# Optimization experiments

Measured on AMD Instinct MI355X. Metric: run time of the kernel, lower is better.

Reference implementation:

```python
import jax, jax.numpy as jnp
import numpy as np

B, T, V, E, H = 64, 32, 32000, 512, 1024  # batch, caption len, vocab, embed, hidden


def setup_inputs() -> dict:
    key = jax.random.key(0)
    ks = jax.random.split(key, 10)
    sV = 1.0 / np.sqrt(V)   # nn.Linear init scale
    sH = 1.0 / np.sqrt(H)   # nn.LSTM init scale
    return {
        "features": jax.random.normal(ks[0], (B, E), jnp.float32),
        "captions": jax.random.randint(ks[1], (B, T), 0, V, dtype=jnp.int32),
        # embed = nn.Linear(vocab_size, embed_size): W [E, V], b [E]
        "W_embed": jax.random.uniform(ks[2], (E, V), jnp.float32, -sV, sV),
        "b_embed": jax.random.uniform(ks[3], (E,), jnp.float32, -sV, sV),
        # single-layer LSTM params, PyTorch gate order (i, f, g, o)
        "w_ih": jax.random.uniform(ks[4], (4 * H, E), jnp.float32, -sH, sH),
        "w_hh": jax.random.uniform(ks[5], (4 * H, H), jnp.float32, -sH, sH),
        "b_ih": jax.random.uniform(ks[6], (4 * H,), jnp.float32, -sH, sH),
        "b_hh": jax.random.uniform(ks[7], (4 * H,), jnp.float32, -sH, sH),
        # the torch module draws these with torch.randn at every call; made explicit here
        "h0": jax.random.normal(ks[8], (B, H), jnp.float32),
        "c0": jax.random.normal(ks[9], (B, H), jnp.float32),
    }


def _lstm(inputs, h0, c0, w_ih, w_hh, b_ih, b_hh):
    # inputs: [B, S, E] -> outputs [B, S, H]
    def step(carry, x_t):
        h, c = carry
        gates = x_t @ w_ih.T + h @ w_hh.T + (b_ih + b_hh)  # [B, 4H]
        i, f, g, o = jnp.split(gates, 4, axis=-1)
        c = jax.nn.sigmoid(f) * c + jax.nn.sigmoid(i) * jnp.tanh(g)
        h = jax.nn.sigmoid(o) * jnp.tanh(c)
        return (h, c), h

    _, hs = jax.lax.scan(step, (h0, c0), jnp.transpose(inputs, (1, 0, 2)))
    return jnp.transpose(hs, (1, 0, 2))


def reference(features, captions, W_embed, b_embed, w_ih, w_hh, b_ih, b_hh, h0, c0):
    # Faithful to the original: expand captions to dense one-hot [B, T, V]
    # and push through the Linear layer (the exact wasteful op pattern under study).
    onehot = jax.nn.one_hot(captions, V, dtype=jnp.float32)       # [B, T, V]
    emb = jnp.einsum("btv,ev->bte", onehot, W_embed) + b_embed     # [B, T, E]
    inputs = jnp.concatenate([features[:, None, :], emb], axis=1)  # [B, T+1, E]
    return _lstm(inputs, h0, c0, w_ih, w_hh, b_ih, b_hh)           # [B, T+1, H]
```

## Files before the change

kernel.cpp:

```cpp
#include <hip/hip_runtime.h>
#include <hip/hip_bf16.h>

#define B_   64
#define T_   32
#define S_   33
#define V_   32000
#define E_   512
#define H_   1024
#define HB_  (B_ * H_)

typedef __attribute__((ext_vector_type(8))) short  bf16x8;
typedef __attribute__((ext_vector_type(4))) float  f32x4;

__device__ inline void split2(float x, unsigned short& hi, unsigned short& lo) {
    __hip_bfloat16 h = __float2bfloat16(x);
    float r = x - __bfloat162float(h);
    __hip_bfloat16 l = __float2bfloat16(r);
    hi = *reinterpret_cast<unsigned short*>(&h);
    lo = *reinterpret_cast<unsigned short*>(&l);
}

__device__ inline void load_f32x8_hilo(const float* __restrict__ p,
                                       bf16x8& hi, bf16x8& lo) {
    const float4* q = reinterpret_cast<const float4*>(p);
    float4 v0 = q[0], v1 = q[1];
    float f[8] = {v0.x, v0.y, v0.z, v0.w, v1.x, v1.y, v1.z, v1.w};
#pragma unroll
    for (int j = 0; j < 8; ++j) {
        unsigned short h, l; split2(f[j], h, l);
        hi[j] = (short)h; lo[j] = (short)l;
    }
}

__device__ inline void load_hpk8(const unsigned int* __restrict__ p,
                                 bf16x8& hi, bf16x8& lo) {
    uint4 v0 = *reinterpret_cast<const uint4*>(p);
    uint4 v1 = *reinterpret_cast<const uint4*>(p + 4);
    unsigned int w[8] = {v0.x, v0.y, v0.z, v0.w, v1.x, v1.y, v1.z, v1.w};
#pragma unroll
    for (int j = 0; j < 8; ++j) {
        hi[j] = (short)(w[j] & 0xffffu);
        lo[j] = (short)(w[j] >> 16);
    }
}

__global__ __launch_bounds__(512) void build_x(
    const float* __restrict__ feat,
    const int*   __restrict__ caps,
    const float* __restrict__ Wemb,
    const float* __restrict__ bemb,
    unsigned short* __restrict__ Xhi,
    unsigned short* __restrict__ Xlo)
{
    int row = blockIdx.x;
    int t = row >> 6, b = row & 63;
    int e = threadIdx.x;
    float x;
    if (t == 0) {
        x = feat[b * E_ + e];
    } else {
        int cap = caps[b * T_ + (t - 1)];
        x = Wemb[(size_t)e * V_ + cap] + bemb[e];
    }
    unsigned short hi, lo; split2(x, hi, lo);
    Xhi[(size_t)row * E_ + e] = hi;
    Xlo[(size_t)row * E_ + e] = lo;
}

__global__ __launch_bounds__(256) void init_state(
    const float* __restrict__ h0,
    const float* __restrict__ c0,
    unsigned int* __restrict__ hseq0,
    float* __restrict__ c,
    unsigned int* __restrict__ flags,
    unsigned int* __restrict__ gen)
{
    int idx = blockIdx.x * 256 + threadIdx.x;
    if (idx < 512 * 32) flags[idx] = 0u;
    if (idx < 128)      gen[idx]   = 0u;
    unsigned short hi, lo; split2(h0[idx], hi, lo);
    hseq0[idx] = (unsigned int)hi | ((unsigned int)lo << 16);
    c[idx]   = c0[idx];
}

__global__ __launch_bounds__(256) void split_w(
    const float* __restrict__ src,
    unsigned short* __restrict__ hi,
    unsigned short* __restrict__ lo,
    int n4)
{
    int idx = blockIdx.x * 256 + threadIdx.x;
    int stride = gridDim.x * 256;
    for (; idx < n4; idx += stride) {
        float4 v = reinterpret_cast<const float4*>(src)[idx];
        float f[4] = {v.x, v.y, v.z, v.w};
        unsigned short h[4], l[4];
#pragma unroll
        for (int j = 0; j < 4; ++j) split2(f[j], h[j], l[j]);
        ushort4 hv; hv.x = h[0]; hv.y = h[1]; hv.z = h[2]; hv.w = h[3];
        ushort4 lv; lv.x = l[0]; lv.y = l[1]; lv.z = l[2]; lv.w = l[3];
        *reinterpret_cast<ushort4*>(hi + (size_t)idx * 4) = hv;
        *reinterpret_cast<ushort4*>(lo + (size_t)idx * 4) = lv;
    }
}

__global__ __launch_bounds__(256) void bias_sum(
    const float* __restrict__ a, const float* __restrict__ b,
    float* __restrict__ s)
{
    int i = blockIdx.x * 256 + threadIdx.x;
    s[i] = a[i] + b[i];
}

template<bool PRESPLIT>
__global__ __launch_bounds__(384, 3) void lstm_persist(
    const unsigned short* __restrict__ Xhi,
    const unsigned short* __restrict__ Xlo,
    const unsigned short* __restrict__ Wihhi,
    const unsigned short* __restrict__ Wihlo,
    const unsigned short* __restrict__ Whhhi,
    const unsigned short* __restrict__ Whhlo,
    const float* __restrict__ w_ih,
    const float* __restrict__ w_hh,
    const float* __restrict__ bsum,
    unsigned int* __restrict__ hseq,
    float* __restrict__ c,
    float* __restrict__ out,
    unsigned int* __restrict__ flags,
    unsigned int* __restrict__ gen)
{
    int bx   = blockIdx.x;
    int jg   = bx & 255;
    int mgrp = bx >> 8;
    int wave = threadIdx.x >> 6;
    int lane = threadIdx.x & 63;
    int lm   = lane & 15;
    int kq   = (lane >> 4) * 8;
    int tid  = threadIdx.x;

    int gbase    = bx & 256;
    bool checker = (bx == gbase);
    unsigned int* mygen = gen + (mgrp * 64);

    int nrow = (lm >> 2) * H_ + jg * 4 + (lm & 3);

    bool xp  = (wave < 2);
    int k0   = xp ? wave * 256 : (wave - 2) * 256;
    const unsigned short* Bhi = nullptr;
    const unsigned short* Blo = nullptr;
    const float* Bf = nullptr;
    if (PRESPLIT) {
        Bhi = xp ? (Wihhi + (size_t)nrow * E_) : (Whhhi + (size_t)nrow * H_);
        Blo = xp ? (Wihlo + (size_t)nrow * E_) : (Whhlo + (size_t)nrow * H_);
    } else {
        Bf  = xp ? (w_ih + (size_t)nrow * E_)  : (w_hh + (size_t)nrow * H_);
    }

    __shared__ float pbuf[6][2][16][17];
    __shared__ float gbuf[2][16][17];
    int rbase = (lane >> 4) * 4;

    for (int t = 0; t < S_; ++t) {
        const unsigned int* hpk_in = hseq + (size_t)t * HB_;
        unsigned int*      hpk_out = hseq + (size_t)(t + 1) * HB_;

        const unsigned short* Axhi = Xhi + (size_t)(t * 64 + mgrp * 32) * E_;
        const unsigned short* Axlo = Xlo + (size_t)(t * 64 + mgrp * 32) * E_;
        const unsigned int* hrow0 = hpk_in + (size_t)(mgrp * 32 + lm) * H_;
        const unsigned int* hrow1 = hpk_in + (size_t)(mgrp * 32 + 16 + lm) * H_;

        f32x4 acc0 = f32x4{0.f, 0.f, 0.f, 0.f};
        f32x4 acc1 = f32x4{0.f, 0.f, 0.f, 0.f};

#pragma unroll
        for (int kk = 0; kk < 256; kk += 32) {
            int k = k0 + kk + kq;
            bf16x8 bhi, blo;
            if constexpr (PRESPLIT) {
                bhi = *reinterpret_cast<const bf16x8*>(Bhi + k);
                blo = *reinterpret_cast<const bf16x8*>(Blo + k);
            } else {
                load_f32x8_hilo(Bf + k, bhi, blo);
            }
            bf16x8 a0h, a0l, a1h, a1l;
            if (xp) {
                a0h = *reinterpret_cast<const bf16x8*>(Axhi + (size_t)lm * E_ + k);
                a0l = *reinterpret_cast<const bf16x8*>(Axlo + (size_t)lm * E_ + k);
                a1h = *reinterpret_cast<const bf16x8*>(Axhi + (size_t)(16 + lm) * E_ + k);
                a1l = *reinterpret_cast<const bf16x8*>(Axlo + (size_t)(16 + lm) * E_ + k);
            } else {
                load_hpk8(hrow0 + k, a0h, a0l);
                load_hpk8(hrow1 + k, a1h, a1l);
            }
            acc0 = __builtin_amdgcn_mfma_f32_16x16x32_bf16(a0h, bhi, acc0, 0, 0, 0);
            acc0 = __builtin_amdgcn_mfma_f32_16x16x32_bf16(a0l, bhi, acc0, 0, 0, 0);
            acc0 = __builtin_amdgcn_mfma_f32_16x16x32_bf16(a0h, blo, acc0, 0, 0, 0);
            acc1 = __builtin_amdgcn_mfma_f32_16x16x32_bf16(a1h, bhi, acc1, 0, 0, 0);
            acc1 = __builtin_amdgcn_mfma_f32_16x16x32_bf16(a1l, bhi, acc1, 0, 0, 0);
            acc1 = __builtin_amdgcn_mfma_f32_16x16x32_bf16(a1h, blo, acc1, 0, 0, 0);
        }

#pragma unroll
        for (int r = 0; r < 4; ++r) {
            pbuf[wave][0][rbase + r][lm] = acc0[r];
            pbuf[wave][1][rbase + r][lm] = acc1[r];
        }
        __syncthreads();

        for (int idx = tid; idx < 512; idx += 384) {
            int mt = idx >> 8, rc = idx & 255;
            int row = rc >> 4, col = rc & 15;
            float v = pbuf[0][mt][row][col] + pbuf[1][mt][row][col]
                    + pbuf[2][mt][row][col] + pbuf[3][mt][row][col]
                    + pbuf[4][mt][row][col] + pbuf[5][mt][row][col];
            int n = (col >> 2) * H_ + jg * 4 + (col & 3);
            gbuf[mt][row][col] = v + bsum[n];
        }
        __syncthreads();

        if (tid < 128) {
            int mt = tid >> 6, bl = (tid >> 2) & 15, jj = tid & 3;
            int b = mgrp * 32 + mt * 16 + bl;
            int j = jg * 4 + jj;
            float iv = gbuf[mt][bl][ 0 + jj];
            float fv = gbuf[mt][bl][ 4 + jj];
            float gv = gbuf[mt][bl][ 8 + jj];
            float ov = gbuf[mt][bl][12 + jj];
            float si = 1.f / (1.f + expf(-iv));
            float sf = 1.f / (1.f + expf(-fv));
            float so = 1.f / (1.f + expf(-ov));
            float tg = tanhf(gv);
            size_t cidx = (size_t)b * H_ + j;
            float cn = sf * c[cidx] + si * tg;
            c[cidx] = cn;
            float hn = so * tanhf(cn);
            unsigned short hi, lo; split2(hn, hi, lo);
            __hip_atomic_store(&hpk_out[cidx],
                               (unsigned int)hi | ((unsigned int)lo << 16),
                               __ATOMIC_RELAXED, __HIP_MEMORY_SCOPE_AGENT);
            out[((size_t)b * S_ + t) * H_ + j] = hn;
        }

        __syncthreads();
        unsigned int target = (unsigned int)(t + 1);
        if (!checker) {
            if (tid == 0) {
                __hip_atomic_store(&flags[(size_t)bx * 32], target,
                                   __ATOMIC_RELAXED, __HIP_MEMORY_SCOPE_AGENT);
                while (__hip_atomic_load(mygen, __ATOMIC_RELAXED,
                                         __HIP_MEMORY_SCOPE_AGENT) < target) {
                    __builtin_amdgcn_s_sleep(2);
                }
            }
        } else {
            int fi = gbase + 1 + tid;
            bool need = (tid < 255);
            for (;;) {
                int ok = 1;
                if (need) {
                    ok = (__hip_atomic_load(&flags[(size_t)fi * 32],
                                            __ATOMIC_RELAXED,
                                            __HIP_MEMORY_SCOPE_AGENT) >= target);
                }
                if (__syncthreads_and(ok)) break;
                __builtin_amdgcn_s_sleep(2);
            }
            if (tid == 0) {
                __hip_atomic_store(mygen, target,
                                   __ATOMIC_RELAXED, __HIP_MEMORY_SCOPE_AGENT);
            }
        }
        __syncthreads();
    }
}

template<bool PRESPLIT>
__global__ __launch_bounds__(384) void lstm_step(
    const unsigned short* __restrict__ Xhi,
    const unsigned short* __restrict__ Xlo,
    const float* __restrict__ w_ih,
    const float* __restrict__ w_hh,
    const unsigned short* __restrict__ Wihhi,
    const unsigned short* __restrict__ Wihlo,
    const unsigned short* __restrict__ Whhhi,
    const unsigned short* __restrict__ Whhlo,
    const float* __restrict__ bsum,
    const unsigned int* __restrict__ hpk_in,
    float* __restrict__ c,
    unsigned int* __restrict__ hpk_out,
    float* __restrict__ out,
    int t)
{
    int bx   = blockIdx.x;
    int jg   = bx & 255;
    int mgrp = bx >> 8;
    int wave = threadIdx.x >> 6;
    int lane = threadIdx.x & 63;
    int lm   = lane & 15;
    int kq   = (lane >> 4) * 8;
    int nrow = (lm >> 2) * H_ + jg * 4 + (lm & 3);

    bool xp  = (wave < 2);
    int k0   = xp ? wave * 256 : (wave - 2) * 256;
    const unsigned short* Bhi = nullptr;
    const unsigned short* Blo = nullptr;
    const float* Bf = nullptr;
    if (PRESPLIT) {
        Bhi = xp ? (Wihhi + (size_t)nrow * E_) : (Whhhi + (size_t)nrow * H_);
        Blo = xp ? (Wihlo + (size_t)nrow * E_) : (Whhlo + (size_t)nrow * H_);
    } else {
        Bf  = xp ? (w_ih + (size_t)nrow * E_)  : (w_hh + (size_t)nrow * H_);
    }
    const unsigned short* Axhi = Xhi + (size_t)(t * 64 + mgrp * 32) * E_;
    const unsigned short* Axlo = Xlo + (size_t)(t * 64 + mgrp * 32) * E_;
    const unsigned int* hrow0 = hpk_in + (size_t)(mgrp * 32 + lm) * H_;
    const unsigned int* hrow1 = hpk_in + (size_t)(mgrp * 32 + 16 + lm) * H_;

    f32x4 acc0 = f32x4{0.f, 0.f, 0.f, 0.f};
    f32x4 acc1 = f32x4{0.f, 0.f, 0.f, 0.f};

#pragma unroll
    for (int kk = 0; kk < 256; kk += 32) {
        int k = k0 + kk + kq;
        bf16x8 bhi, blo;
        if constexpr (PRESPLIT) {
            bhi = *reinterpret_cast<const bf16x8*>(Bhi + k);
            blo = *reinterpret_cast<const bf16x8*>(Blo + k);
        } else {
            load_f32x8_hilo(Bf + k, bhi, blo);
        }
        bf16x8 a0h, a0l, a1h, a1l;
        if (xp) {
            a0h = *reinterpret_cast<const bf16x8*>(Axhi + (size_t)lm * E_ + k);
            a0l = *reinterpret_cast<const bf16x8*>(Axlo + (size_t)lm * E_ + k);
            a1h = *reinterpret_cast<const bf16x8*>(Axhi + (size_t)(16 + lm) * E_ + k);
            a1l = *reinterpret_cast<const bf16x8*>(Axlo + (size_t)(16 + lm) * E_ + k);
        } else {
            load_hpk8(hrow0 + k, a0h, a0l);
            load_hpk8(hrow1 + k, a1h, a1l);
        }
        acc0 = __builtin_amdgcn_mfma_f32_16x16x32_bf16(a0h, bhi, acc0, 0, 0, 0);
        acc0 = __builtin_amdgcn_mfma_f32_16x16x32_bf16(a0l, bhi, acc0, 0, 0, 0);
        acc0 = __builtin_amdgcn_mfma_f32_16x16x32_bf16(a0h, blo, acc0, 0, 0, 0);
        acc1 = __builtin_amdgcn_mfma_f32_16x16x32_bf16(a1h, bhi, acc1, 0, 0, 0);
        acc1 = __builtin_amdgcn_mfma_f32_16x16x32_bf16(a1l, bhi, acc1, 0, 0, 0);
        acc1 = __builtin_amdgcn_mfma_f32_16x16x32_bf16(a1h, blo, acc1, 0, 0, 0);
    }

    __shared__ float pbuf[6][2][16][17];
    __shared__ float gbuf[2][16][17];
    int rbase = (lane >> 4) * 4;
#pragma unroll
    for (int r = 0; r < 4; ++r) {
        pbuf[wave][0][rbase + r][lm] = acc0[r];
        pbuf[wave][1][rbase + r][lm] = acc1[r];
    }
    __syncthreads();

    int tid = threadIdx.x;
    for (int idx = tid; idx < 512; idx += 384) {
        int mt = idx >> 8, rc = idx & 255;
        int row = rc >> 4, col = rc & 15;
        float v = pbuf[0][mt][row][col] + pbuf[1][mt][row][col]
                + pbuf[2][mt][row][col] + pbuf[3][mt][row][col]
                + pbuf[4][mt][row][col] + pbuf[5][mt][row][col];
        int n = (col >> 2) * H_ + jg * 4 + (col & 3);
        gbuf[mt][row][col] = v + bsum[n];
    }
    __syncthreads();

    if (tid < 128) {
        int mt = tid >> 6, bl = (tid >> 2) & 15, jj = tid & 3;
        int b = mgrp * 32 + mt * 16 + bl;
        int j = jg * 4 + jj;
        float iv = gbuf[mt][bl][ 0 + jj];
        float fv = gbuf[mt][bl][ 4 + jj];
        float gv = gbuf[mt][bl][ 8 + jj];
        float ov = gbuf[mt][bl][12 + jj];
        float si = 1.f / (1.f + expf(-iv));
        float sf = 1.f / (1.f + expf(-fv));
        float so = 1.f / (1.f + expf(-ov));
        float tg = tanhf(gv);
        size_t cidx = (size_t)b * H_ + j;
        float cn = sf * c[cidx] + si * tg;
        c[cidx] = cn;
        float hn = so * tanhf(cn);
        unsigned short hi, lo; split2(hn, hi, lo);
        hpk_out[cidx] = (unsigned int)hi | ((unsigned int)lo << 16);
        out[((size_t)b * S_ + t) * H_ + j] = hn;
    }
}

extern "C" void kernel_launch(void* const* d_in, const int* in_sizes, int n_in,
                              void* d_out, int out_size, void* d_ws, size_t ws_size,
                              hipStream_t stream)
{
    const float* feat = (const float*)d_in[0];
    const int*   caps = (const int*)d_in[1];
    const float* Wemb = (const float*)d_in[2];
    const float* bemb = (const float*)d_in[3];
    const float* w_ih = (const float*)d_in[4];
    const float* w_hh = (const float*)d_in[5];
    const float* b_ih = (const float*)d_in[6];
    const float* b_hh = (const float*)d_in[7];
    const float* h0   = (const float*)d_in[8];
    const float* c0   = (const float*)d_in[9];
    int nbias = 0, nstate = 0;
    for (int i = 0; i < n_in; ++i) {
        switch (in_sizes[i]) {
            case 64 * 512:        feat = (const float*)d_in[i]; break;
            case 64 * 32:         caps = (const int*)d_in[i];   break;
            case 512 * 32000:     Wemb = (const float*)d_in[i]; break;
            case 512:             bemb = (const float*)d_in[i]; break;
            case 4096 * 512:      w_ih = (const float*)d_in[i]; break;
            case 4096 * 1024:     w_hh = (const float*)d_in[i]; break;
            case 4096:
                if (nbias++ == 0) b_ih = (const float*)d_in[i];
                else              b_hh = (const float*)d_in[i];
                break;
            case 64 * 1024:
                if (nstate++ == 0) h0 = (const float*)d_in[i];
                else               c0 = (const float*)d_in[i];
                break;
            default: break;
        }
    }
    float* out = (float*)d_out;

    char* ws = (char*)d_ws;
    unsigned short* Xhi  = (unsigned short*)ws; ws += (size_t)2112 * 512 * 2;
    unsigned short* Xlo  = (unsigned short*)ws; ws += (size_t)2112 * 512 * 2;
    unsigned int* hseq   = (unsigned int*)ws;   ws += (size_t)(S_ + 1) * HB_ * 4;
    float* cbuf          = (float*)ws;          ws += (size_t)B_ * H_ * 4;
    float* bsum          = (float*)ws;          ws += (size_t)4096 * 4;
    unsigned int* flags  = (unsigned int*)ws;   ws += (size_t)512 * 32 * 4;
    unsigned int* gen    = (unsigned int*)ws;   ws += (size_t)128 * 4;
    unsigned short* Wihhi = (unsigned short*)ws; ws += (size_t)4096 * 512 * 2;
    unsigned short* Wihlo = (unsigned short*)ws; ws += (size_t)4096 * 512 * 2;
    unsigned short* Whhhi = (unsigned short*)ws; ws += (size_t)4096 * 1024 * 2;
    unsigned short* Whhlo = (unsigned short*)ws; ws += (size_t)4096 * 1024 * 2;
    size_t needed = (size_t)(ws - (char*)d_ws);
    bool presplit = ws_size >= needed;

    build_x<<<2112, 512, 0, stream>>>(feat, caps, Wemb, bemb, Xhi, Xlo);
    init_state<<<256, 256, 0, stream>>>(h0, c0, hseq, cbuf, flags, gen);
    bias_sum<<<16, 256, 0, stream>>>(b_ih, b_hh, bsum);
    if (presplit) {
        split_w<<<2048, 256, 0, stream>>>(w_ih, Wihhi, Wihlo, (4096 * 512) / 4);
        split_w<<<2048, 256, 0, stream>>>(w_hh, Whhhi, Whhlo, (4096 * 1024) / 4);
    }

    void* args[] = {
        (void*)&Xhi, (void*)&Xlo,
        (void*)&Wihhi, (void*)&Wihlo, (void*)&Whhhi, (void*)&Whhlo,
        (void*)&w_ih, (void*)&w_hh,
        (void*)&bsum,
        (void*)&hseq,
        (void*)&cbuf, (void*)&out, (void*)&flags, (void*)&gen
    };
    const void* pk = presplit ? (const void*)lstm_persist<true>
                              : (const void*)lstm_persist<false>;
    hipError_t err = hipLaunchCooperativeKernel(pk, dim3(512), dim3(384),
                                                args, 0, stream);
    if (err != hipSuccess) {
        (void)hipGetLastError();
        for (int t = 0; t < S_; ++t) {
            const unsigned int* hin = hseq + (size_t)t * HB_;
            unsigned int*      hout = hseq + (size_t)(t + 1) * HB_;
            if (presplit) {
                lstm_step<true><<<512, 384, 0, stream>>>(
                    Xhi, Xlo, w_ih, w_hh, Wihhi, Wihlo, Whhhi, Whhlo, bsum,
                    hin, cbuf, hout, out, t);
            } else {
                lstm_step<false><<<512, 384, 0, stream>>>(
                    Xhi, Xlo, w_ih, w_hh, Wihhi, Wihlo, Whhhi, Whhlo, bsum,
                    hin, cbuf, hout, out, t);
            }
        }
    }
}
```

Baseline: 736.5 us.

## Hoist input-to-hidden projection out of recurrent loop into batched GEMM

Computes x_t·W_ih^T plus bias for all timesteps in a separate parallel GEMM kernel before the recurrence, storing the gate preactivations in a workspace buffer. The persistent LSTM kernel now only does the h·W_hh^T product per step, using 4 waves instead of 6, and adds the precomputed input gates when applying the nonlinearities. This takes a third of the per-step matmul work off the serial critical path. In exchange it adds an extra kernel launch and roughly 35 MB of extra workspace traffic.

```diff
diff --git a/kernel.cpp b/kernel.cpp
--- a/kernel.cpp
+++ b/kernel.cpp
@@ -8,6 +8,7 @@
 #define E_   512
 #define H_   1024
 #define HB_  (B_ * H_)
+#define NG_  4096
 
 typedef __attribute__((ext_vector_type(8))) short  bf16x8;
 typedef __attribute__((ext_vector_type(4))) float  f32x4;
@@ -113,16 +114,82 @@
 }
 
 template<bool PRESPLIT>
-__global__ __launch_bounds__(384, 3) void lstm_persist(
+__global__ __launch_bounds__(256) void gx_gemm(
     const unsigned short* __restrict__ Xhi,
     const unsigned short* __restrict__ Xlo,
     const unsigned short* __restrict__ Wihhi,
     const unsigned short* __restrict__ Wihlo,
+    const float* __restrict__ w_ih,
+    const float* __restrict__ bsum,
+    float* __restrict__ Gxi)
+{
+    int bx   = blockIdx.x;
+    int jg   = bx & 255;
+    int m0   = (bx >> 8) * 32;
+    int wave = threadIdx.x >> 6;
+    int lane = threadIdx.x & 63;
+    int lm   = lane & 15;
+    int kq   = (lane >> 4) * 8;
+    int tid  = threadIdx.x;
+    int nrow = (lm >> 2) * H_ + jg * 4 + (lm & 3);
+    int k0   = wave * 128;
+
+    const unsigned short* Bhi = nullptr;
+    const unsigned short* Blo = nullptr;
+    const float* Bf = nullptr;
+    if (PRESPLIT) { Bhi = Wihhi + (size_t)nrow * E_; Blo = Wihlo + (size_t)nrow * E_; }
+    else          { Bf  = w_ih + (size_t)nrow * E_; }
+
+    f32x4 acc0 = f32x4{0.f, 0.f, 0.f, 0.f};
+    f32x4 acc1 = f32x4{0.f, 0.f, 0.f, 0.f};
+
+#pragma unroll
+    for (int kk = 0; kk < 128; kk += 32) {
+        int k = k0 + kk + kq;
+        bf16x8 bhi, blo;
+        if constexpr (PRESPLIT) {
+            bhi = *reinterpret_cast<const bf16x8*>(Bhi + k);
+            blo = *reinterpret_cast<const bf16x8*>(Blo + k);
+        } else {
+            load_f32x8_hilo(Bf + k, bhi, blo);
+        }
+        bf16x8 a0h = *reinterpret_cast<const bf16x8*>(Xhi + (size_t)(m0 + lm) * E_ + k);
+        bf16x8 a0l = *reinterpret_cast<const bf16x8*>(Xlo + (size_t)(m0 + lm) * E_ + k);
+        bf16x8 a1h = *reinterpret_cast<const bf16x8*>(Xhi + (size_t)(m0 + 16 + lm) * E_ + k);
+        bf16x8 a1l = *reinterpret_cast<const bf16x8*>(Xlo + (size_t)(m0 + 16 + lm) * E_ + k);
+        acc0 = __builtin_amdgcn_mfma_f32_16x16x32_bf16(a0h, bhi, acc0, 0, 0, 0);
+        acc0 = __builtin_amdgcn_mfma_f32_16x16x32_bf16(a0l, bhi, acc0, 0, 0, 0);
+        acc0 = __builtin_amdgcn_mfma_f32_16x16x32_bf16(a0h, blo, acc0, 0, 0, 0);
+        acc1 = __builtin_amdgcn_mfma_f32_16x16x32_bf16(a1h, bhi, acc1, 0, 0, 0);
+        acc1 = __builtin_amdgcn_mfma_f32_16x16x32_bf16(a1l, bhi, acc1, 0, 0, 0);
+        acc1 = __builtin_amdgcn_mfma_f32_16x16x32_bf16(a1h, blo, acc1, 0, 0, 0);
+    }
+
+    __shared__ float pbuf[4][2][16][17];
+    int rbase = (lane >> 4) * 4;
+#pragma unroll
+    for (int r = 0; r < 4; ++r) {
+        pbuf[wave][0][rbase + r][lm] = acc0[r];
+        pbuf[wave][1][rbase + r][lm] = acc1[r];
+    }
+    __syncthreads();
+
+    for (int idx = tid; idx < 512; idx += 256) {
+        int mt = idx >> 8, rc = idx & 255;
+        int row = rc >> 4, col = rc & 15;
+        float v = pbuf[0][mt][row][col] + pbuf[1][mt][row][col]
+                + pbuf[2][mt][row][col] + pbuf[3][mt][row][col];
+        int n = (col >> 2) * H_ + jg * 4 + (col & 3);
+        Gxi[(size_t)(m0 + mt * 16 + row) * NG_ + jg * 16 + col] = v + bsum[n];
+    }
+}
+
+template<bool PRESPLIT>
+__global__ __launch_bounds__(256, 2) void lstm_persist(
+    const float* __restrict__ Gxi,
     const unsigned short* __restrict__ Whhhi,
     const unsigned short* __restrict__ Whhlo,
-    const float* __restrict__ w_ih,
     const float* __restrict__ w_hh,
-    const float* __restrict__ bsum,
     unsigned int* __restrict__ hseq,
     float* __restrict__ c,
     float* __restrict__ out,
@@ -143,29 +210,21 @@
     unsigned int* mygen = gen + (mgrp * 64);
 
     int nrow = (lm >> 2) * H_ + jg * 4 + (lm & 3);
-
-    bool xp  = (wave < 2);
-    int k0   = xp ? wave * 256 : (wave - 2) * 256;
+    int k0   = wave * 256;
+
     const unsigned short* Bhi = nullptr;
     const unsigned short* Blo = nullptr;
     const float* Bf = nullptr;
-    if (PRESPLIT) {
-        Bhi = xp ? (Wihhi + (size_t)nrow * E_) : (Whhhi + (size_t)nrow * H_);
-        Blo = xp ? (Wihlo + (size_t)nrow * E_) : (Whhlo + (size_t)nrow * H_);
-    } else {
-        Bf  = xp ? (w_ih + (size_t)nrow * E_)  : (w_hh + (size_t)nrow * H_);
-    }
-
-    __shared__ float pbuf[6][2][16][17];
+    if (PRESPLIT) { Bhi = Whhhi + (size_t)nrow * H_; Blo = Whhlo + (size_t)nrow * H_; }
+    else          { Bf  = w_hh + (size_t)nrow * H_; }
+
+    __shared__ float pbuf[4][2][16][17];
     __shared__ float gbuf[2][16][17];
     int rbase = (lane >> 4) * 4;
 
     for (int t = 0; t < S_; ++t) {
         const unsigned int* hpk_in = hseq + (size_t)t * HB_;
         unsigned int*      hpk_out = hseq + (size_t)(t + 1) * HB_;
-
-        const unsigned short* Axhi = Xhi + (size_t)(t * 64 + mgrp * 32) * E_;
-        const unsigned short* Axlo = Xlo + (size_t)(t * 64 + mgrp * 32) * E_;
         const unsigned int* hrow0 = hpk_in + (size_t)(mgrp * 32 + lm) * H_;
         const unsigned int* hrow1 = hpk_in + (size_t)(mgrp * 32 + 16 + lm) * H_;
 
@@ -183,15 +242,8 @@
                 load_f32x8_hilo(Bf + k, bhi, blo);
             }
             bf16x8 a0h, a0l, a1h, a1l;
-            if (xp) {
-                a0h = *reinterpret_cast<const bf16x8*>(Axhi + (size_t)lm * E_ + k);
-                a0l = *reinterpret_cast<const bf16x8*>(Axlo + (size_t)lm * E_ + k);
-                a1h = *reinterpret_cast<const bf16x8*>(Axhi + (size_t)(16 + lm) * E_ + k);
-                a1l = *reinterpret_cast<const bf16x8*>(Axlo + (size_t)(16 + lm) * E_ + k);
-            } else {
-                load_hpk8(hrow0 + k, a0h, a0l);
-                load_hpk8(hrow1 + k, a1h, a1l);
-            }
+            load_hpk8(hrow0 + k, a0h, a0l);
+            load_hpk8(hrow1 + k, a1h, a1l);
             acc0 = __builtin_amdgcn_mfma_f32_16x16x32_bf16(a0h, bhi, acc0, 0, 0, 0);
             acc0 = __builtin_amdgcn_mfma_f32_16x16x32_bf16(a0l, bhi, acc0, 0, 0, 0);
             acc0 = __builtin_amdgcn_mfma_f32_16x16x32_bf16(a0h, blo, acc0, 0, 0, 0);
@@ -207,14 +259,11 @@
         }
         __syncthreads();
 
-        for (int idx = tid; idx < 512; idx += 384) {
+        for (int idx = tid; idx < 512; idx += 256) {
             int mt = idx >> 8, rc = idx & 255;
             int row = rc >> 4, col = rc & 15;
-            float v = pbuf[0][mt][row][col] + pbuf[1][mt][row][col]
-                    + pbuf[2][mt][row][col] + pbuf[3][mt][row][col]
-                    + pbuf[4][mt][row][col] + pbuf[5][mt][row][col];
-            int n = (col >> 2) * H_ + jg * 4 + (col & 3);
-            gbuf[mt][row][col] = v + bsum[n];
+            gbuf[mt][row][col] = pbuf[0][mt][row][col] + pbuf[1][mt][row][col]
+                               + pbuf[2][mt][row][col] + pbuf[3][mt][row][col];
         }
         __syncthreads();
 
@@ -222,10 +271,11 @@
             int mt = tid >> 6, bl = (tid >> 2) & 15, jj = tid & 3;
             int b = mgrp * 32 + mt * 16 + bl;
             int j = jg * 4 + jj;
-            float iv = gbuf[mt][bl][ 0 + jj];
-            float fv = gbuf[mt][bl][ 4 + jj];
-            float gv = gbuf[mt][bl][ 8 + jj];
-            float ov = gbuf[mt][bl][12 + jj];
+            const float* gx = Gxi + (size_t)(t * 64 + b) * NG_ + jg * 16;
+            float iv = gbuf[mt][bl][ 0 + jj] + gx[ 0 + jj];
+            float fv = gbuf[mt][bl][ 4 + jj] + gx[ 4 + jj];
+            float gv = gbuf[mt][bl][ 8 + jj] + gx[ 8 + jj];
+            float ov = gbuf[mt][bl][12 + jj] + gx[12 + jj];
             float si = 1.f / (1.f + expf(-iv));
             float sf = 1.f / (1.f + expf(-fv));
             float so = 1.f / (1.f + expf(-ov));
@@ -275,16 +325,11 @@
 }
 
 template<bool PRESPLIT>
-__global__ __launch_bounds__(384) void lstm_step(
-    const unsigned short* __restrict__ Xhi,
-    const unsigned short* __restrict__ Xlo,
-    const float* __restrict__ w_ih,
-    const float* __restrict__ w_hh,
-    const unsigned short* __restrict__ Wihhi,
-    const unsigned short* __restrict__ Wihlo,
+__global__ __launch_bounds__(256) void lstm_step(
+    const float* __restrict__ Gxi,
     const unsigned short* __restrict__ Whhhi,
     const unsigned short* __restrict__ Whhlo,
-    const float* __restrict__ bsum,
+    const float* __restrict__ w_hh,
     const unsigned int* __restrict__ hpk_in,
     float* __restrict__ c,
     unsigned int* __restrict__ hpk_out,
@@ -298,21 +343,16 @@
     int lane = threadIdx.x & 63;
     int lm   = lane & 15;
     int kq   = (lane >> 4) * 8;
+    int tid  = threadIdx.x;
     int nrow = (lm >> 2) * H_ + jg * 4 + (lm & 3);
-
-    bool xp  = (wave < 2);
-    int k0   = xp ? wave * 256 : (wave - 2) * 256;
+    int k0   = wave * 256;
+
     const unsigned short* Bhi = nullptr;
     const unsigned short* Blo = nullptr;
     const float* Bf = nullptr;
-    if (PRESPLIT) {
-        Bhi = xp ? (Wihhi + (size_t)nrow * E_) : (Whhhi + (size_t)nrow * H_);
-        Blo = xp ? (Wihlo + (size_t)nrow * E_) : (Whhlo + (size_t)nrow * H_);
-    } else {
-        Bf  = xp ? (w_ih + (size_t)nrow * E_)  : (w_hh + (size_t)nrow * H_);
-    }
-    const unsigned short* Axhi = Xhi + (size_t)(t * 64 + mgrp * 32) * E_;
-    const unsigned short* Axlo = Xlo + (size_t)(t * 64 + mgrp * 32) * E_;
+    if (PRESPLIT) { Bhi = Whhhi + (size_t)nrow * H_; Blo = Whhlo + (size_t)nrow * H_; }
+    else          { Bf  = w_hh + (size_t)nrow * H_; }
+
     const unsigned int* hrow0 = hpk_in + (size_t)(mgrp * 32 + lm) * H_;
     const unsigned int* hrow1 = hpk_in + (size_t)(mgrp * 32 + 16 + lm) * H_;
 
@@ -330,15 +370,8 @@
             load_f32x8_hilo(Bf + k, bhi, blo);
         }
         bf16x8 a0h, a0l, a1h, a1l;
-        if (xp) {
-            a0h = *reinterpret_cast<const bf16x8*>(Axhi + (size_t)lm * E_ + k);
-            a0l = *reinterpret_cast<const bf16x8*>(Axlo + (size_t)lm * E_ + k);
-            a1h = *reinterpret_cast<const bf16x8*>(Axhi + (size_t)(16 + lm) * E_ + k);
-            a1l = *reinterpret_cast<const bf16x8*>(Axlo + (size_t)(16 + lm) * E_ + k);
-        } else {
-            load_hpk8(hrow0 + k, a0h, a0l);
-            load_hpk8(hrow1 + k, a1h, a1l);
-        }
+        load_hpk8(hrow0 + k, a0h, a0l);
+        load_hpk8(hrow1 + k, a1h, a1l);
         acc0 = __builtin_amdgcn_mfma_f32_16x16x32_bf16(a0h, bhi, acc0, 0, 0, 0);
         acc0 = __builtin_amdgcn_mfma_f32_16x16x32_bf16(a0l, bhi, acc0, 0, 0, 0);
         acc0 = __builtin_amdgcn_mfma_f32_16x16x32_bf16(a0h, blo, acc0, 0, 0, 0);
@@ -347,7 +380,7 @@
         acc1 = __builtin_amdgcn_mfma_f32_16x16x32_bf16(a1h, blo, acc1, 0, 0, 0);
     }
 
-    __shared__ float pbuf[6][2][16][17];
+    __shared__ float pbuf[4][2][16][17];
     __shared__ float gbuf[2][16][17];
     int rbase = (lane >> 4) * 4;
 #pragma unroll
@@ -357,15 +390,11 @@
     }
     __syncthreads();
 
-    int tid = threadIdx.x;
-    for (int idx = tid; idx < 512; idx += 384) {
+    for (int idx = tid; idx < 512; idx += 256) {
         int mt = idx >> 8, rc = idx & 255;
         int row = rc >> 4, col = rc & 15;
-        float v = pbuf[0][mt][row][col] + pbuf[1][mt][row][col]
-                + pbuf[2][mt][row][col] + pbuf[3][mt][row][col]
-                + pbuf[4][mt][row][col] + pbuf[5][mt][row][col];
-        int n = (col >> 2) * H_ + jg * 4 + (col & 3);
-        gbuf[mt][row][col] = v + bsum[n];
+        gbuf[mt][row][col] = pbuf[0][mt][row][col] + pbuf[1][mt][row][col]
+                           + pbuf[2][mt][row][col] + pbuf[3][mt][row][col];
     }
     __syncthreads();
 
@@ -373,10 +402,11 @@
         int mt = tid >> 6, bl = (tid >> 2) & 15, jj = tid & 3;
         int b = mgrp * 32 + mt * 16 + bl;
         int j = jg * 4 + jj;
-        float iv = gbuf[mt][bl][ 0 + jj];
-        float fv = gbuf[mt][bl][ 4 + jj];
-        float gv = gbuf[mt][bl][ 8 + jj];
-        float ov = gbuf[mt][bl][12 + jj];
+        const float* gx = Gxi + (size_t)(t * 64 + b) * NG_ + jg * 16;
+        float iv = gbuf[mt][bl][ 0 + jj] + gx[ 0 + jj];
+        float fv = gbuf[mt][bl][ 4 + jj] + gx[ 4 + jj];
+        float gv = gbuf[mt][bl][ 8 + jj] + gx[ 8 + jj];
+        float ov = gbuf[mt][bl][12 + jj] + gx[12 + jj];
         float si = 1.f / (1.f + expf(-iv));
         float sf = 1.f / (1.f + expf(-fv));
         float so = 1.f / (1.f + expf(-ov));
@@ -430,6 +460,7 @@
     char* ws = (char*)d_ws;
     unsigned short* Xhi  = (unsigned short*)ws; ws += (size_t)2112 * 512 * 2;
     unsigned short* Xlo  = (unsigned short*)ws; ws += (size_t)2112 * 512 * 2;
+    float* Gxi           = (float*)ws;          ws += (size_t)2112 * NG_ * 4;
     unsigned int* hseq   = (unsigned int*)ws;   ws += (size_t)(S_ + 1) * HB_ * 4;
     float* cbuf          = (float*)ws;          ws += (size_t)B_ * H_ * 4;
     float* bsum          = (float*)ws;          ws += (size_t)4096 * 4;
@@ -448,19 +479,22 @@
     if (presplit) {
         split_w<<<2048, 256, 0, stream>>>(w_ih, Wihhi, Wihlo, (4096 * 512) / 4);
         split_w<<<2048, 256, 0, stream>>>(w_hh, Whhhi, Whhlo, (4096 * 1024) / 4);
+        gx_gemm<true><<<66 * 256, 256, 0, stream>>>(Xhi, Xlo, Wihhi, Wihlo,
+                                                    w_ih, bsum, Gxi);
+    } else {
+        gx_gemm<false><<<66 * 256, 256, 0, stream>>>(Xhi, Xlo, Wihhi, Wihlo,
+                                                     w_ih, bsum, Gxi);
     }
 
     void* args[] = {
-        (void*)&Xhi, (void*)&Xlo,
-        (void*)&Wihhi, (void*)&Wihlo, (void*)&Whhhi, (void*)&Whhlo,
-        (void*)&w_ih, (void*)&w_hh,
-        (void*)&bsum,
-        (void*)&hseq,
-        (void*)&cbuf, (void*)&out, (void*)&flags, (void*)&gen
+        (void*)&Gxi,
+        (void*)&Whhhi, (void*)&Whhlo, (void*)&w_hh,
+        (void*)&hseq, (void*)&cbuf, (void*)&out,
+        (void*)&flags, (void*)&gen
     };
     const void* pk = presplit ? (const void*)lstm_persist<true>
                               : (const void*)lstm_persist<false>;
-    hipError_t err = hipLaunchCooperativeKernel(pk, dim3(512), dim3(384),
+    hipError_t err = hipLaunchCooperativeKernel(pk, dim3(512), dim3(256),
                                                 args, 0, stream);
     if (err != hipSuccess) {
         (void)hipGetLastError();
@@ -468,13 +502,11 @@
             const unsigned int* hin = hseq + (size_t)t * HB_;
             unsigned int*      hout = hseq + (size_t)(t + 1) * HB_;
             if (presplit) {
-                lstm_step<true><<<512, 384, 0, stream>>>(
-                    Xhi, Xlo, w_ih, w_hh, Wihhi, Wihlo, Whhhi, Whhlo, bsum,
-                    hin, cbuf, hout, out, t);
+                lstm_step<true><<<512, 256, 0, stream>>>(
+                    Gxi, Whhhi, Whhlo, w_hh, hin, cbuf, hout, out, t);
             } else {
-                lstm_step<false><<<512, 384, 0, stream>>>(
-                    Xhi, Xlo, w_ih, w_hh, Wihhi, Wihlo, Whhhi, Whhlo, bsum,
-                    hin, cbuf, hout, out, t);
+                lstm_step<false><<<512, 256, 0, stream>>>(
+                    Gxi, Whhhi, Whhlo, w_hh, hin, cbuf, hout, out, t);
             }
         }
     }
```

Result: faster. 720.3 us (-2.2%).
